# Kernel optimization log

Measured on AMD Instinct MI355X. Metric: run time of the kernel, lower is better.

## Reference

```python
import jax, jax.numpy as jnp
import numpy as np
from math import factorial

# ---------- Clebsch-Gordan coefficients (e3nn real-basis convention) ----------
def _su2_cg(j1, m1, j2, m2, j3, m3):
    if m3 != m1 + m2:
        return 0.0
    f = factorial
    vmin = int(max(-j1 + j2 + m3, -j1 + m1, 0))
    vmax = int(min(j2 + j3 + m1, j3 - j1 + j2, j3 + m3))
    c = ((2 * j3 + 1) * f(j3 + j1 - j2) * f(j3 - j1 + j2) * f(j1 + j2 - j3) / f(j1 + j2 + j3 + 1)
         * f(j3 + m3) * f(j3 - m3) / (f(j1 + m1) * f(j1 - m1) * f(j2 + m2) * f(j2 - m2))) ** 0.5
    s = 0.0
    for v in range(vmin, vmax + 1):
        s += (-1.0) ** (v + j2 + m2) / f(v) * f(j2 + j3 + m1 - v) * f(j1 - m1 + v) \
             / f(j3 - j1 + j2 - v) / f(j3 + m3 - v) / f(v + j1 - j2 - m3)
    return c * s

def _q(l):
    # change of basis real -> complex spherical harmonics, with (-i)^l phase (e3nn)
    q = np.zeros((2 * l + 1, 2 * l + 1), dtype=np.complex128)
    for m in range(-l, 0):
        q[l + m, l + abs(m)] = 2 ** -0.5
        q[l + m, l - abs(m)] = -1j * 2 ** -0.5
    q[l, l] = 1.0
    for m in range(1, l + 1):
        q[l + m, l + abs(m)] = (-1) ** m * 2 ** -0.5
        q[l + m, l - abs(m)] = 1j * (-1) ** m * 2 ** -0.5
    return (-1j) ** l * q

def _w3j(l1, l2, l3):
    # real-basis Wigner 3j, unit Frobenius norm (e3nn convention)
    C = np.zeros((2 * l1 + 1, 2 * l2 + 1, 2 * l3 + 1), dtype=np.complex128)
    for m1 in range(-l1, l1 + 1):
        for m2 in range(-l2, l2 + 1):
            m3 = m1 + m2
            if abs(m3) <= l3:
                C[l1 + m1, l2 + m2, l3 + m3] = _su2_cg(l1, m1, l2, m2, l3, m3)
    C = np.einsum('ij,kl,mn,ikm->jln', _q(l1), _q(l2), np.conj(_q(l3)), C).real
    return (C / np.linalg.norm(C)).astype(np.float32)

MAX_ELL = 3
AVG_NEIGH = 16.0
P_ENV = 6
N_NODES = 2048
MUL = 64

# tensor-product paths (l1 from Y=0e+1o+2e+3o, l2 from V=0e+1o+2e),
# filtered to ir_out in {0e,1o,2e} (= '0e' + output_irreps), grouped by output ir
PATHS_0E = [(0, 0, 0), (1, 1, 0), (2, 2, 0)]
PATHS_1O = [(0, 1, 1), (1, 0, 1), (1, 2, 1), (2, 1, 1), (3, 2, 1)]
PATHS_2E = [(0, 2, 2), (1, 1, 2), (2, 0, 2), (2, 2, 2), (3, 1, 2)]
_CG = {p: _w3j(*p) for p in PATHS_0E + PATHS_1O + PATHS_2E}
_CG_REC = [_w3j(1, 1, 2), _w3j(2, 1, 3)]  # for SH recursion

def _sh_scales():
    # component normalization: ||Y_l(n)|| = sqrt(2l+1) for unit n
    n = np.array([0.3, 0.5, 0.81]); n /= np.linalg.norm(n)
    nyzx = np.array([n[1], n[2], n[0]])
    Y = np.sqrt(3.0) * nyzx
    scales = []
    for i, l in enumerate((1, 2)):
        A = np.einsum('i,j,ijk->k', Y, nyzx, _CG_REC[i])
        s = np.sqrt(2 * (l + 1) + 1.0) / np.linalg.norm(A)
        scales.append(np.float32(s))
        Y = A * s
    return scales
_SH_SCALES = _sh_scales()

def _sph(vectors):
    # component-normalized real spherical harmonics l=0..3 (e3nn y,z,x basis)
    n = vectors / jnp.linalg.norm(vectors, axis=-1, keepdims=True)
    nyzx = jnp.stack([n[:, 1], n[:, 2], n[:, 0]], axis=-1)
    Y0 = jnp.ones((vectors.shape[0], 1), vectors.dtype)
    Y1 = np.float32(np.sqrt(3.0)) * nyzx
    Y2 = _SH_SCALES[0] * jnp.einsum('ei,ej,ijk->ek', Y1, nyzx, _CG_REC[0])
    Y3 = _SH_SCALES[1] * jnp.einsum('ei,ej,ijk->ek', Y2, nyzx, _CG_REC[1])
    return jnp.concatenate([Y0, Y1, Y2, Y3], axis=-1)  # (E, 16)

def _compute_silu_c():
    # e3nn normalized activation: silu(z) / sqrt(E[silu(z)^2]), z~N(0,1)
    trapz = getattr(np, 'trapezoid', getattr(np, 'trapz', None))
    z = np.linspace(-12.0, 12.0, 200001)
    phi = np.exp(-z * z / 2) / np.sqrt(2 * np.pi)
    s = z / (1.0 + np.exp(-z))
    return np.float32(1.0 / np.sqrt(trapz(s * s * phi, z)))
_SILU_C = _compute_silu_c()

def _silu_n(x):
    return jax.nn.silu(x) * _SILU_C

def _sl(l):
    return slice(l * l, (l + 1) * (l + 1))

def _envelope(d, p=P_ENV):
    # e3nn poly_envelope(p-1, 2) == DimeNet cutoff polynomial
    a = np.float32(-(p + 1) * (p + 2) / 2)
    b = np.float32(p * (p + 2))
    c = np.float32(-p * (p + 1) / 2)
    val = 1.0 + a * d ** p + b * d ** (p + 1) + c * d ** (p + 2)
    return jnp.where(d < 1.0, val, jnp.zeros_like(d))

def _forward(vectors, x, V, senders, W0, W1, W2, W3, Wl1, Wl2):
    E = x.shape[0]
    # edge-wise channel weights: mlp((mul_gcd,), act=None)
    w = (x @ W0) * np.float32(1.0 / np.sqrt(x.shape[1]))          # (E, MUL)
    Y = _sph(vectors)                                              # (E, 16)
    wY = w[:, :, None] * Y[:, None, :]                             # (E, MUL, 16)
    node_sum = jax.ops.segment_sum(wY, senders, num_segments=N_NODES)
    wY = node_sum[senders] * np.float32(1.0 / np.sqrt(AVG_NEIGH))  # scatter_sum(map_back=True)
    Vc = V.reshape(E, MUL, 9)                                      # mul_to_axis: 0e+1o+2e

    def tp(paths):
        outs = [np.float32(np.sqrt(2 * l3 + 1)) *
                jnp.einsum('eui,euj,ijk->euk', wY[:, :, _sl(l1)], Vc[:, :, _sl(l2)], _CG[(l1, l2, l3)])
                for (l1, l2, l3) in paths]
        return jnp.stack(outs, axis=2)  # (E, MUL, n_paths, 2*l3+1)

    s0 = tp(PATHS_0E).reshape(E, MUL * 3)      # 192x0e scalars
    v1 = tp(PATHS_1O).reshape(E, MUL * 5, 3)   # 320x1o
    v2 = tp(PATHS_2E).reshape(E, MUL * 5, 5)   # 320x2e

    # scalar track: concat 0e outputs, 3-layer MLP (normalized silu, no output act)
    x2 = jnp.concatenate([x, s0], axis=1)
    h = _silu_n(x2 @ W1 * np.float32(1.0 / np.sqrt(x2.shape[1])))
    h = _silu_n(h @ W2 * np.float32(1.0 / np.sqrt(h.shape[1])))
    h = h @ W3 * np.float32(1.0 / np.sqrt(h.shape[1]))
    d = jnp.linalg.norm(vectors, axis=-1, keepdims=True)
    x_out = _envelope(d) * h                                       # (E, 64)

    # equivariant track: e3nn Linear to 64x0e+64x1o+64x2e (no 0e input -> zeros)
    inv = np.float32(1.0 / np.sqrt(MUL * 5))
    o1 = jnp.einsum('emi,mu->eui', v1, Wl1) * inv
    o2 = jnp.einsum('emi,mu->eui', v2, Wl2) * inv
    V_out = jnp.concatenate([jnp.zeros((E, MUL), x.dtype),
                             o1.reshape(E, MUL * 3), o2.reshape(E, MUL * 5)], axis=1)  # (E, 576)
    return x_out, V_out

def setup_inputs() -> dict:
    key = jax.random.key(0)
    ks = jax.random.split(key, 11)
    E, XD = 32768, 128
    v = jax.random.normal(ks[0], (E, 3), dtype=jnp.float32)
    r = jax.random.uniform(ks[1], (E, 1), minval=0.05, maxval=0.95, dtype=jnp.float32)
    vectors = v / jnp.linalg.norm(v, axis=1, keepdims=True) * r  # lengths in (0,1): inside cutoff
    return {
        'vectors': vectors,
        'x': jax.random.normal(ks[2], (E, XD), dtype=jnp.float32),
        'V': jax.random.normal(ks[3], (E, MUL * 9), dtype=jnp.float32),
        'senders': jax.random.randint(ks[4], (E,), 0, N_NODES),
        'W0': jax.random.normal(ks[5], (XD, MUL), dtype=jnp.float32),
        'W1': jax.random.normal(ks[6], (XD + 3 * MUL, 64), dtype=jnp.float32),
        'W2': jax.random.normal(ks[7], (64, 64), dtype=jnp.float32),
        'W3': jax.random.normal(ks[8], (64, 64), dtype=jnp.float32),
        'Wl1': jax.random.normal(ks[9], (5 * MUL, MUL), dtype=jnp.float32),
        'Wl2': jax.random.normal(ks[10], (5 * MUL, MUL), dtype=jnp.float32),
    }

def reference(vectors, x, V, senders, W0, W1, W2, W3, Wl1, Wl2):
    return _forward(vectors, x, V, senders, W0, W1, W2, W3, Wl1, Wl2)
```

## Files before the change

### kernel.cpp

```cpp
#include <hip/hip_runtime.h>
#include <cmath>
#include <utility>

#define DI __device__ __forceinline__

typedef __attribute__((ext_vector_type(8))) short  short8;
typedef __attribute__((ext_vector_type(4))) float  f32x4;

constexpr double cfact(int n){ double r=1.0; for(int i=2;i<=n;++i) r*=(double)i; return r; }
constexpr double csqrt(double x){ if(x<=0.0) return 0.0; double g = x>1.0?x:1.0; for(int i=0;i<100;++i) g = 0.5*(g + x/g); return g; }
constexpr double csgn(int k){ int m = k%2; if(m<0) m+=2; return m? -1.0:1.0; }
constexpr int cmax3(int a,int b,int c){ int m=a>b?a:b; return m>c?m:c; }
constexpr int cmin3(int a,int b,int c){ int m=a<b?a:b; return m<c?m:c; }

struct cplx { double r, i; };
constexpr cplx cmul(cplx a, cplx b){ return cplx{a.r*b.r - a.i*b.i, a.r*b.i + a.i*b.r}; }
constexpr cplx cadd(cplx a, cplx b){ return cplx{a.r+b.r, a.i+b.i}; }
constexpr cplx cscale(cplx a, double s){ return cplx{a.r*s, a.i*s}; }
constexpr cplx cconj(cplx a){ return cplx{a.r, -a.i}; }

constexpr double su2_cg(int j1,int m1,int j2,int m2,int j3,int m3){
  if (m3 != m1+m2) return 0.0;
  const int vmin = cmax3(-j1+j2+m3, -j1+m1, 0);
  const int vmax = cmin3(j2+j3+m1, j3-j1+j2, j3+m3);
  const double c = csqrt((2.0*j3+1.0) * cfact(j3+j1-j2)*cfact(j3-j1+j2)*cfact(j1+j2-j3)/cfact(j1+j2+j3+1)
                         * cfact(j3+m3)*cfact(j3-m3)
                         / (cfact(j1+m1)*cfact(j1-m1)*cfact(j2+m2)*cfact(j2-m2)));
  double s = 0.0;
  for (int v=vmin; v<=vmax; ++v){
    s += csgn(v+j2+m2)/cfact(v)*cfact(j2+j3+m1-v)*cfact(j1-m1+v)
         /cfact(j3-j1+j2-v)/cfact(j3+m3-v)/cfact(v+j1-j2-m3);
  }
  return c*s;
}

template<int L> struct QM { cplx v[2*L+1][2*L+1]; };
template<int L> constexpr QM<L> qmat(){
  QM<L> q{};
  const double is2 = 0.70710678118654752440;
  for (int m=-L; m<0; ++m){
    q.v[L+m][L-m] = cplx{is2, 0.0};
    q.v[L+m][L+m] = cplx{0.0, -is2};
  }
  q.v[L][L] = cplx{1.0, 0.0};
  for (int m=1; m<=L; ++m){
    const double sg = (m%2)? -1.0 : 1.0;
    q.v[L+m][L+m] = cplx{sg*is2, 0.0};
    q.v[L+m][L-m] = cplx{0.0, sg*is2};
  }
  const cplx ph = (L%4==0)?cplx{1,0} : (L%4==1)?cplx{0,-1} : (L%4==2)?cplx{-1,0} : cplx{0,1};
  for (int a=0;a<2*L+1;++a) for(int b=0;b<2*L+1;++b) q.v[a][b] = cmul(ph, q.v[a][b]);
  return q;
}

template<int L1,int L2,int L3> struct W3J { float v[2*L1+1][2*L2+1][2*L3+1]; };

template<int L1,int L2,int L3> constexpr W3J<L1,L2,L3> w3j(){
  constexpr int N1=2*L1+1, N2=2*L2+1, N3=2*L3+1;
  double C[N1][N2][N3] = {};
  for (int m1=-L1;m1<=L1;++m1) for (int m2=-L2;m2<=L2;++m2){
    const int m3=m1+m2;
    if (m3>=-L3 && m3<=L3) C[L1+m1][L2+m2][L3+m3] = su2_cg(L1,m1,L2,m2,L3,m3);
  }
  const QM<L1> q1 = qmat<L1>(); const QM<L2> q2 = qmat<L2>(); const QM<L3> q3 = qmat<L3>();
  cplx T1[N1][N2][N3] = {};
  for(int j=0;j<N1;++j) for(int k=0;k<N2;++k) for(int m=0;m<N3;++m){
    cplx acc{0,0};
    for(int i=0;i<N1;++i) acc = cadd(acc, cscale(q1.v[i][j], C[i][k][m]));
    T1[j][k][m]=acc;
  }
  cplx T2[N1][N2][N3] = {};
  for(int j=0;j<N1;++j) for(int l=0;l<N2;++l) for(int m=0;m<N3;++m){
    cplx acc{0,0};
    for(int k=0;k<N2;++k) acc = cadd(acc, cmul(q2.v[k][l], T1[j][k][m]));
    T2[j][l][m]=acc;
  }
  double O[N1][N2][N3] = {};
  double fro = 0.0;
  for(int j=0;j<N1;++j) for(int l=0;l<N2;++l) for(int n=0;n<N3;++n){
    cplx acc{0,0};
    for(int m=0;m<N3;++m) acc = cadd(acc, cmul(cconj(q3.v[m][n]), T2[j][l][m]));
    O[j][l][n] = acc.r;
    fro += acc.r*acc.r;
  }
  const double inv = 1.0/csqrt(fro);
  W3J<L1,L2,L3> w{};
  for(int j=0;j<N1;++j) for(int l=0;l<N2;++l) for(int n=0;n<N3;++n)
    w.v[j][l][n] = (float)(O[j][l][n]*inv);
  return w;
}

constexpr auto CG_000 = w3j<0,0,0>();
constexpr auto CG_110 = w3j<1,1,0>();
constexpr auto CG_220 = w3j<2,2,0>();
constexpr auto CG_011 = w3j<0,1,1>();
constexpr auto CG_101 = w3j<1,0,1>();
constexpr auto CG_121 = w3j<1,2,1>();
constexpr auto CG_211 = w3j<2,1,1>();
constexpr auto CG_321 = w3j<3,2,1>();
constexpr auto CG_022 = w3j<0,2,2>();
constexpr auto CG_112 = w3j<1,1,2>();
constexpr auto CG_202 = w3j<2,0,2>();
constexpr auto CG_222 = w3j<2,2,2>();
constexpr auto CG_312 = w3j<3,1,2>();
constexpr auto CG_213 = w3j<2,1,3>();

struct ShS { double s0, s1; };
constexpr ShS sh_scales(){
  const double n0=0.3,n1=0.5,n2=0.81;
  const double nn = csqrt(n0*n0+n1*n1+n2*n2);
  const double ny[3] = {n1/nn, n2/nn, n0/nn};
  const double sq3 = csqrt(3.0);
  double Y1[3]; for(int i=0;i<3;++i) Y1[i] = sq3*ny[i];
  double A[5] = {};
  for(int i=0;i<3;++i) for(int j=0;j<3;++j) for(int k=0;k<5;++k)
    A[k] += Y1[i]*ny[j]*(double)CG_112.v[i][j][k];
  double na=0; for(int k=0;k<5;++k) na += A[k]*A[k]; na = csqrt(na);
  const double s0 = csqrt(5.0)/na;
  double Y2[5]; for(int k=0;k<5;++k) Y2[k] = A[k]*s0;
  double B[7] = {};
  for(int i=0;i<5;++i) for(int j=0;j<3;++j) for(int k=0;k<7;++k)
    B[k] += Y2[i]*ny[j]*(double)CG_213.v[i][j][k];
  double nb=0; for(int k=0;k<7;++k) nb += B[k]*B[k]; nb = csqrt(nb);
  const double s1 = csqrt(7.0)/nb;
  return ShS{s0,s1};
}
constexpr ShS SHS = sh_scales();

template<typename F, int... Is>
DI void sfor_impl(F&& f, std::integer_sequence<int, Is...>){ (f(std::integral_constant<int,Is>{}), ...); }
template<int N, typename F>
DI void sfor(F&& f){ sfor_impl(f, std::make_integer_sequence<int, N>{}); }

template<int N>
__host__ __device__ constexpr bool col_any(const float (&c)[N]){
  for(int k=0;k<N;++k) if (c[k]!=0.0f) return true;
  return false;
}

#define CONTRACT3(TAB, NI, NJ, NK, SCALE, INI, INJ, OUT) \
  sfor<(NI)>([&](auto I__){ constexpr int i__ = decltype(I__)::value; \
    sfor<(NJ)>([&](auto J__){ constexpr int j__ = decltype(J__)::value; \
      if constexpr (col_any((TAB).v[i__][j__])) { \
        const float t__ = (INI)[i__] * (INJ)[j__]; \
        sfor<(NK)>([&](auto K__){ constexpr int k__ = decltype(K__)::value; \
          if constexpr ((TAB).v[i__][j__][k__] != 0.0f) { \
            constexpr float c__ = (float)((double)(TAB).v[i__][j__][k__] * (double)(SCALE)); \
            (OUT)[k__] = fmaf(c__, t__, (OUT)[k__]); \
          } }); } }); });

DI unsigned short f2bf(float f){
  unsigned int u = __float_as_uint(f);
  u += 0x7fffu + ((u >> 16) & 1u);
  return (unsigned short)(u >> 16);
}
DI float silu_n(float z, float c){ return c * (z / (1.0f + __expf(-z))); }

constexpr float SQRT3F        = (float)csqrt(3.0);
constexpr double SQ3D         = csqrt(3.0);
constexpr double SQ5D         = csqrt(5.0);
constexpr float INV_SQRT_XD   = (float)(1.0/csqrt(128.0));
constexpr float INV_SQRT_NEI  = 0.25f;
constexpr float INV320        = (float)(1.0/csqrt(320.0));

constexpr int E_TOT = 32768;
constexpr int NNODE = 2048;

DI short8 load_bfrag_raw(const float* __restrict__ W, int kt, int nt, int lane){
  const int q = lane >> 4, c = lane & 15;
  const float* src = W + (kt*32 + q*8)*64 + nt*16 + c;
  short8 b;
  #pragma unroll
  for (int j=0;j<8;++j) b[j] = (short)f2bf(src[j*64]);
  return b;
}

__global__ __launch_bounds__(256) void k_setup(
    const int* __restrict__ senders, int* __restrict__ pos, int* __restrict__ cnt,
    const float* __restrict__ W0, const float* __restrict__ W1,
    const float* __restrict__ Wl1, const float* __restrict__ Wl2,
    const float* __restrict__ W2, const float* __restrict__ W3,
    short8* __restrict__ bfrag)
{
  const int blk = blockIdx.x;
  if (blk < 38){
    if (bfrag == nullptr) return;
    const int wv = threadIdx.x >> 6, lane = threadIdx.x & 63;
    const int wid = blk*4 + wv;
    if (wid >= 152) return;
    const float* W; int kt, nt;
    if (wid < 16){ W = W0; kt = wid>>2; nt = wid&3; }
    else if (wid < 136){ const int t = wid-16; const int mat = t/40, r = t%40;
           W = (mat==0)?W1 : (mat==1)?Wl1 : Wl2; kt = r>>2; nt = r&3; }
    else { const int t = wid-136; const int r = t&7;
           W = (t<8)?W2:W3; kt = r>>2; nt = r&3; }
    bfrag[wid*64 + lane] = load_bfrag_raw(W, kt, nt, lane);
  } else {
    const int e = (blk-38)*256 + threadIdx.x;
    if (e < E_TOT) pos[e] = atomicAdd(&cnt[senders[e]], 1);
  }
}

__global__ __launch_bounds__(256) void k_scan(const int* __restrict__ cnt, int* __restrict__ off)
{
  __shared__ int ts[256];
  const int t = threadIdx.x;
  int loc[8]; int s = 0;
  #pragma unroll
  for (int i=0;i<8;++i){ int v = cnt[t*8+i]; loc[i] = s; s += v; }
  ts[t] = s;
  __syncthreads();
  int val = s;
  for (int d=1; d<256; d<<=1){
    int other = (t>=d)? ts[t-d] : 0;
    __syncthreads();
    val += other; ts[t] = val;
    __syncthreads();
  }
  const int base = val - s;
  #pragma unroll
  for (int i=0;i<8;++i) off[t*8+i] = base + loc[i];
  if (t==255) off[2048] = val;
}

__global__ __launch_bounds__(256) void k_wy(
    const float* __restrict__ vectors, const float* __restrict__ x,
    const int* __restrict__ senders, const float* __restrict__ W0,
    const int* __restrict__ pos, const int* __restrict__ off,
    const short8* __restrict__ bfrag,
    float* __restrict__ w_un, float* __restrict__ Y_un, int* __restrict__ eids)
{
  const int tid = threadIdx.x, lane = tid & 63, wv = tid >> 6;
  const int e0 = blockIdx.x * 64;
  const int r = lane & 15, q = lane >> 4;
  const int erow = e0 + wv*16 + r;

  f32x4 acc[4] = {{0.f,0.f,0.f,0.f},{0.f,0.f,0.f,0.f},{0.f,0.f,0.f,0.f},{0.f,0.f,0.f,0.f}};
  #pragma unroll
  for (int kt=0; kt<4; ++kt){
    const float4* xp = (const float4*)(x + (size_t)erow*128 + kt*32 + q*8);
    const float4 xa = xp[0], xb = xp[1];
    short8 a;
    a[0]=(short)f2bf(xa.x); a[1]=(short)f2bf(xa.y); a[2]=(short)f2bf(xa.z); a[3]=(short)f2bf(xa.w);
    a[4]=(short)f2bf(xb.x); a[5]=(short)f2bf(xb.y); a[6]=(short)f2bf(xb.z); a[7]=(short)f2bf(xb.w);
    #pragma unroll
    for (int nt=0; nt<4; ++nt){
      const short8 b = (bfrag != nullptr) ? bfrag[(kt*4+nt)*64 + lane]
                                          : load_bfrag_raw(W0, kt, nt, lane);
      acc[nt] = __builtin_amdgcn_mfma_f32_16x16x32_bf16(a, b, acc[nt], 0,0,0);
    }
  }
  #pragma unroll
  for (int nt=0; nt<4; ++nt)
    #pragma unroll
    for (int reg=0; reg<4; ++reg){
      const int row = q*4 + reg;
      w_un[(size_t)(e0 + wv*16 + row)*64 + nt*16 + r] = acc[nt][reg] * INV_SQRT_XD;
    }

  if (tid < 64){
    const int e = e0 + tid;
    const float vx = vectors[e*3+0], vy = vectors[e*3+1], vz = vectors[e*3+2];
    const float dn = sqrtf(vx*vx+vy*vy+vz*vz);
    const float ny[3] = {vy/dn, vz/dn, vx/dn};
    float Y[16];
    Y[0] = 1.f; Y[1] = SQRT3F*ny[0]; Y[2] = SQRT3F*ny[1]; Y[3] = SQRT3F*ny[2];
    #pragma unroll
    for (int k=4;k<16;++k) Y[k] = 0.f;
    CONTRACT3(CG_112, 3,3,5, SHS.s0, (Y+1), ny, (Y+4));
    CONTRACT3(CG_213, 5,3,7, SHS.s1, (Y+4), ny, (Y+9));
    #pragma unroll
    for (int k=0;k<16;++k) Y_un[e*16+k] = Y[k];
    const int s = senders[e];
    eids[off[s] + pos[e]] = e;
  }
}

__global__ __launch_bounds__(256) void k_gather(
    const float* __restrict__ w_un, const float* __restrict__ Y_un,
    const int* __restrict__ off, const int* __restrict__ eids,
    float* __restrict__ node_sum)
{
  const int lane = threadIdx.x & 63;
  const int wv = threadIdx.x >> 6;
  const int n = __builtin_amdgcn_readfirstlane((int)blockIdx.x*4 + wv);
  const int p0 = off[n], p1 = off[n+1];
  float acc[16];
  #pragma unroll
  for (int k=0;k<16;++k) acc[k] = 0.f;
  if (p1 > p0){
    int eid = eids[p0];
    float wu = w_un[(size_t)eid*64 + lane];
    float yv[16];
    #pragma unroll
    for (int k=0;k<16;++k) yv[k] = Y_un[eid*16 + k];
    for (int p=p0+1; p<p1; ++p){
      const int eid2 = eids[p];
      const float wu2 = w_un[(size_t)eid2*64 + lane];
      float yv2[16];
      #pragma unroll
      for (int k=0;k<16;++k) yv2[k] = Y_un[eid2*16 + k];
      #pragma unroll
      for (int k=0;k<16;++k) acc[k] = fmaf(yv[k], wu, acc[k]);
      wu = wu2;
      #pragma unroll
      for (int k=0;k<16;++k) yv[k] = yv2[k];
    }
    #pragma unroll
    for (int k=0;k<16;++k) acc[k] = fmaf(yv[k], wu, acc[k]);
  }
  float* dst = node_sum + n*1024;
  #pragma unroll
  for (int k=0;k<16;++k) dst[k*64 + lane] = acc[k] * INV_SQRT_NEI;
}

DI void wr2(char* AF, int tile, int row, int m, float val){
  const int kt = m >> 5, m0 = m & 31;
  *(unsigned short*)(AF + (((tile*10 + kt)*16 + row)<<6)
                        + ((m0<<1) ^ (((row>>1)&3)<<4))) = f2bf(val);
}

constexpr int SSTR = 580;

__global__ __launch_bounds__(256,5) void k_main(
    const float* __restrict__ vectors, const float* __restrict__ x,
    const float* __restrict__ V, const int* __restrict__ senders,
    const float* __restrict__ W1, const float* __restrict__ W2,
    const float* __restrict__ W3, const float* __restrict__ Wl1,
    const float* __restrict__ Wl2, const float* __restrict__ node_sum,
    const short8* __restrict__ bfrag,
    float* __restrict__ out_x, float* __restrict__ out_V, float silu_c)
{
  __shared__ __align__(16) char smem[30752];
  char*  AF    = smem;
  float* stage = (float*)(smem + 2048);
  char*  h1b   = smem;
  char*  h2b   = smem + 12288;
  float* envs  = (float*)(smem + 30720);

  const int tid  = threadIdx.x;
  const int lane = tid & 63;
  const int wv   = tid >> 6;
  const int blk  = blockIdx.x;

  {
    const int el = wv;
    const int e  = __builtin_amdgcn_readfirstlane(blk*4 + el);
    const int s  = senders[e];
    const int u  = lane;

    float* smV = (float*)(smem + wv*2304);
    #pragma unroll
    for (int j=0;j<9;++j) smV[j*64 + lane] = V[(size_t)e*576 + j*64 + lane];
    float vc[9];
    #pragma unroll
    for (int j=0;j<9;++j) vc[j] = smV[u*9 + j];

    float g[16];
    const float* nsrow = node_sum + s*1024;
    #pragma unroll
    for (int k=0;k<16;++k) g[k] = nsrow[k*64+u];
    const float x0 = x[(size_t)e*128 + u];
    const float x1 = x[(size_t)e*128 + 64 + u];

    const float vx = vectors[e*3+0], vy = vectors[e*3+1], vz = vectors[e*3+2];
    const float d  = sqrtf(vx*vx + vy*vy + vz*vz);
    const float d3 = d*d*d, d6 = d3*d3;
    const float env = (d < 1.f) ? (1.f + d6*(-28.f + d*(48.f + d*(-21.f)))) : 0.f;
    if (lane == 0) envs[wv] = env;

    __syncthreads();

    float s0[3] = {0.f,0.f,0.f};
    float v1o[5][3] = {};
    float v2o[5][5] = {};
    CONTRACT3(CG_000, 1,1,1, 1.0, (g+0), (vc+0), (&s0[0]));
    CONTRACT3(CG_110, 3,3,1, 1.0, (g+1), (vc+1), (&s0[1]));
    CONTRACT3(CG_220, 5,5,1, 1.0, (g+4), (vc+4), (&s0[2]));
    CONTRACT3(CG_011, 1,3,3, SQ3D, (g+0), (vc+1), (v1o[0]));
    CONTRACT3(CG_101, 3,1,3, SQ3D, (g+1), (vc+0), (v1o[1]));
    CONTRACT3(CG_121, 3,5,3, SQ3D, (g+1), (vc+4), (v1o[2]));
    CONTRACT3(CG_211, 5,3,3, SQ3D, (g+4), (vc+1), (v1o[3]));
    CONTRACT3(CG_321, 7,5,3, SQ3D, (g+9), (vc+4), (v1o[4]));
    CONTRACT3(CG_022, 1,5,5, SQ5D, (g+0), (vc+4), (v2o[0]));
    CONTRACT3(CG_112, 3,3,5, SQ5D, (g+1), (vc+1), (v2o[1]));
    CONTRACT3(CG_202, 5,1,5, SQ5D, (g+4), (vc+0), (v2o[2]));
    CONTRACT3(CG_222, 5,5,5, SQ5D, (g+4), (vc+4), (v2o[3]));
    CONTRACT3(CG_312, 7,3,5, SQ5D, (g+9), (vc+1), (v2o[4]));

    wr2(AF, 0, el, u,      x0);
    wr2(AF, 0, el, 64 + u, x1);
    #pragma unroll
    for (int p=0;p<3;++p) wr2(AF, 0, el, 128 + u*3 + p, s0[p]);
    #pragma unroll
    for (int p=0;p<5;++p){
      const int m = u*5 + p;
      #pragma unroll
      for (int i=0;i<3;++i) wr2(AF, 0, 4 + i*4 + el, m, v1o[p][i]);
      #pragma unroll
      for (int i=0;i<4;++i) wr2(AF, 1, i*4 + el, m, v2o[p][i]);
      wr2(AF, 2, el, m, v2o[p][4]);
    }
  }
  __syncthreads();

  f32x4 accS={0.f,0.f,0.f,0.f}, accV1=accS, accA=accS, accB=accS;
  const int nt = wv;
  const int arow = lane & 15;
  const int aoff = arow*64 + (((lane>>4)<<4) ^ (((arow>>1)&3)<<4));
  __builtin_amdgcn_s_setprio(1);
  #pragma unroll 2
  for (int kt=0; kt<10; ++kt){
    short8 b0, b1, b2;
    if (bfrag != nullptr){
      b0 = bfrag[(16 + kt*4 + nt)*64 + lane];
      b1 = bfrag[(56 + kt*4 + nt)*64 + lane];
      b2 = bfrag[(96 + kt*4 + nt)*64 + lane];
    } else {
      b0 = load_bfrag_raw(W1,  kt, nt, lane);
      b1 = load_bfrag_raw(Wl1, kt, nt, lane);
      b2 = load_bfrag_raw(Wl2, kt, nt, lane);
    }
    const char* ab = AF + kt*1024 + aoff;
    const short8 a0 = *(const short8*)(ab);
    const short8 a1 = *(const short8*)(ab + 10240);
    const short8 a2 = *(const short8*)(ab + 20480);
    accS  = __builtin_amdgcn_mfma_f32_16x16x32_bf16(a0, b0, accS,  0,0,0);
    accV1 = __builtin_amdgcn_mfma_f32_16x16x32_bf16(a0, b1, accV1, 0,0,0);
    accA  = __builtin_amdgcn_mfma_f32_16x16x32_bf16(a1, b2, accA,  0,0,0);
    accB  = __builtin_amdgcn_mfma_f32_16x16x32_bf16(a2, b2, accB,  0,0,0);
  }
  __builtin_amdgcn_s_setprio(0);
  __syncthreads();

  const int col = lane & 15, qq = lane >> 4;
  const int u2 = nt*16 + col;
  stage[qq*SSTR + u2] = 0.f;
  #pragma unroll
  for (int reg=0; reg<4; ++reg){
    const int row = qq*4 + reg;
    if (row < 4){
      wr2(h1b, 0, row, u2, silu_n(accS[reg] * INV320, silu_c));
      stage[row*SSTR + 256 + u2*5 + 4] = accB[reg] * INV320;
    } else {
      const int rr = row - 4, i = rr>>2, ee = rr&3;
      stage[ee*SSTR + 64 + u2*3 + i] = accV1[reg] * INV320;
    }
    { const int i2 = row>>2, ee = row&3;
      stage[ee*SSTR + 256 + u2*5 + i2] = accA[reg] * INV320; }
  }
  __syncthreads();

  f32x4 acc2 = {0.f,0.f,0.f,0.f};
  #pragma unroll
  for (int kt2=0; kt2<2; ++kt2){
    const short8 b = (bfrag != nullptr) ? bfrag[(136 + kt2*4 + nt)*64 + lane]
                                        : load_bfrag_raw(W2, kt2, nt, lane);
    const short8 a = *(const short8*)(h1b + kt2*1024 + aoff);
    acc2 = __builtin_amdgcn_mfma_f32_16x16x32_bf16(a, b, acc2, 0,0,0);
  }
  if (qq == 0){
    #pragma unroll
    for (int reg=0; reg<4; ++reg)
      wr2(h2b, 0, reg, u2, silu_n(acc2[reg] * 0.125f, silu_c));
  }
  __syncthreads();

  f32x4 acc3 = {0.f,0.f,0.f,0.f};
  #pragma unroll
  for (int kt2=0; kt2<2; ++kt2){
    const short8 b = (bfrag != nullptr) ? bfrag[(144 + kt2*4 + nt)*64 + lane]
                                        : load_bfrag_raw(W3, kt2, nt, lane);
    const short8 a = *(const short8*)(h2b + kt2*1024 + aoff);
    acc3 = __builtin_amdgcn_mfma_f32_16x16x32_bf16(a, b, acc3, 0,0,0);
  }
  if (qq == 0){
    #pragma unroll
    for (int reg=0; reg<4; ++reg)
      out_x[(size_t)(blk*4 + reg)*64 + u2] = envs[reg] * (acc3[reg] * 0.125f);
  }

  const int e2 = blk*4 + wv;
  const float* st = stage + wv*SSTR;
  #pragma unroll
  for (int j=0;j<9;++j) out_V[(size_t)e2*576 + j*64 + lane] = st[j*64 + lane];
}

static const float g_silu_c = [](){
  const int N = 200001;
  const double h = 24.0/(double)(N-1);
  double acc = 0.0;
  for (int i=0;i<N;++i){
    const double z = -12.0 + h*(double)i;
    const double phi = std::exp(-z*z/2.0)/std::sqrt(2.0*M_PI);
    const double s = z/(1.0+std::exp(-z));
    const double f = s*s*phi;
    acc += (i==0 || i==N-1) ? 0.5*f : f;
  }
  return (float)(1.0/std::sqrt(acc*h));
}();

extern "C" void kernel_launch(void* const* d_in, const int* in_sizes, int n_in,
                              void* d_out, int out_size, void* d_ws, size_t ws_size,
                              hipStream_t stream) {
  (void)in_sizes; (void)n_in; (void)out_size;
  const float* vectors = (const float*)d_in[0];
  const float* x       = (const float*)d_in[1];
  const float* V       = (const float*)d_in[2];
  const int*   senders = (const int*)  d_in[3];
  const float* W0      = (const float*)d_in[4];
  const float* W1      = (const float*)d_in[5];
  const float* W2      = (const float*)d_in[6];
  const float* W3      = (const float*)d_in[7];
  const float* Wl1     = (const float*)d_in[8];
  const float* Wl2     = (const float*)d_in[9];
  float* out_x = (float*)d_out;
  float* out_V = out_x + (size_t)E_TOT*64;

  char* ob = (char*)d_out;
  int*   pos   = (int*)(ob);
  int*   cnt   = (int*)(ob + 131072);
  int*   off   = (int*)(ob + 139264);
  int*   eids  = (int*)(ob + 151552);
  float* w_un  = (float*)(ob + 282624);
  float* Y_un  = (float*)(ob + 282624 + 8388608);

  float* node_sum = (float*)d_ws;
  const size_t WS_NEED = (size_t)8*1024*1024 + 152*1024;
  short8* bfrag = (ws_size >= WS_NEED) ? (short8*)((char*)d_ws + 8*1024*1024) : nullptr;

  hipMemsetAsync(cnt, 0, 8192, stream);
  k_setup <<<dim3(166), dim3(256), 0, stream>>>(senders, pos, cnt, W0, W1, Wl1, Wl2, W2, W3, bfrag);
  k_scan  <<<dim3(1),   dim3(256), 0, stream>>>(cnt, off);
  k_wy    <<<dim3(E_TOT/64), dim3(256), 0, stream>>>(vectors, x, senders, W0, pos, off, bfrag, w_un, Y_un, eids);
  k_gather<<<dim3(NNODE/4),  dim3(256), 0, stream>>>(w_un, Y_un, off, eids, node_sum);
  k_main  <<<dim3(E_TOT/4),  dim3(256), 0, stream>>>(vectors, x, V, senders,
                                                     W1, W2, W3, Wl1, Wl2,
                                                     node_sum, bfrag, out_x, out_V, g_silu_c);
}
```

Baseline: 248.6 us.

## Replace sort-and-gather aggregation with fused atomic scatter into node sums

Drops the counting sort (setup atomics, scan, eid scatter) and the separate gather kernel. One kernel now computes the W0 projection and the spherical harmonics per edge and atomically adds the outer products straight into a zeroed node_sum buffer. Weight fragment preparation moves into extra blocks of that kernel. This removes several launches and the intermediate w_un/Y_un round trip, but issues 1024 float atomics per edge, makes summation order nondeterministic, and reads W0 fragments raw from fp32 in every block.

After: 324.2 us. 1.3x slower.

```diff
diff --git a/kernel.cpp b/kernel.cpp
--- a/kernel.cpp
+++ b/kernel.cpp
@@ -160,8 +160,8 @@
 constexpr double SQ3D         = csqrt(3.0);
 constexpr double SQ5D         = csqrt(5.0);
 constexpr float INV_SQRT_XD   = (float)(1.0/csqrt(128.0));
-constexpr float INV_SQRT_NEI  = 0.25f;
 constexpr float INV320        = (float)(1.0/csqrt(320.0));
+constexpr float WSCALE        = (float)((1.0/csqrt(128.0)) * 0.25);
 
 constexpr int E_TOT = 32768;
 constexpr int NNODE = 2048;
@@ -175,88 +175,37 @@
   return b;
 }
 
-__global__ __launch_bounds__(256) void k_setup(
-    const int* __restrict__ senders, int* __restrict__ pos, int* __restrict__ cnt,
-    const float* __restrict__ W0, const float* __restrict__ W1,
-    const float* __restrict__ Wl1, const float* __restrict__ Wl2,
-    const float* __restrict__ W2, const float* __restrict__ W3,
-    short8* __restrict__ bfrag)
-{
-  const int blk = blockIdx.x;
-  if (blk < 38){
-    if (bfrag == nullptr) return;
-    const int wv = threadIdx.x >> 6, lane = threadIdx.x & 63;
-    const int wid = blk*4 + wv;
-    if (wid >= 152) return;
-    const float* W; int kt, nt;
-    if (wid < 16){ W = W0; kt = wid>>2; nt = wid&3; }
-    else if (wid < 136){ const int t = wid-16; const int mat = t/40, r = t%40;
-           W = (mat==0)?W1 : (mat==1)?Wl1 : Wl2; kt = r>>2; nt = r&3; }
-    else { const int t = wid-136; const int r = t&7;
-           W = (t<8)?W2:W3; kt = r>>2; nt = r&3; }
-    bfrag[wid*64 + lane] = load_bfrag_raw(W, kt, nt, lane);
-  } else {
-    const int e = (blk-38)*256 + threadIdx.x;
-    if (e < E_TOT) pos[e] = atomicAdd(&cnt[senders[e]], 1);
-  }
-}
-
-__global__ __launch_bounds__(256) void k_scan(const int* __restrict__ cnt, int* __restrict__ off)
-{
-  __shared__ int ts[256];
-  const int t = threadIdx.x;
-  int loc[8]; int s = 0;
-  #pragma unroll
-  for (int i=0;i<8;++i){ int v = cnt[t*8+i]; loc[i] = s; s += v; }
-  ts[t] = s;
-  __syncthreads();
-  int val = s;
-  for (int d=1; d<256; d<<=1){
-    int other = (t>=d)? ts[t-d] : 0;
-    __syncthreads();
-    val += other; ts[t] = val;
-    __syncthreads();
-  }
-  const int base = val - s;
-  #pragma unroll
-  for (int i=0;i<8;++i) off[t*8+i] = base + loc[i];
-  if (t==255) off[2048] = val;
-}
-
-__global__ __launch_bounds__(256) void k_wy(
+__global__ __launch_bounds__(256) void k_scat(
     const float* __restrict__ vectors, const float* __restrict__ x,
     const int* __restrict__ senders, const float* __restrict__ W0,
-    const int* __restrict__ pos, const int* __restrict__ off,
-    const short8* __restrict__ bfrag,
-    float* __restrict__ w_un, float* __restrict__ Y_un, int* __restrict__ eids)
+    const float* __restrict__ W1, const float* __restrict__ Wl1,
+    const float* __restrict__ Wl2, const float* __restrict__ W2,
+    const float* __restrict__ W3,
+    short8* __restrict__ bfrag, float* __restrict__ node_sum)
 {
   const int tid = threadIdx.x, lane = tid & 63, wv = tid >> 6;
-  const int e0 = blockIdx.x * 64;
-  const int r = lane & 15, q = lane >> 4;
-  const int erow = e0 + wv*16 + r;
-
-  f32x4 acc[4] = {{0.f,0.f,0.f,0.f},{0.f,0.f,0.f,0.f},{0.f,0.f,0.f,0.f},{0.f,0.f,0.f,0.f}};
-  #pragma unroll
-  for (int kt=0; kt<4; ++kt){
-    const float4* xp = (const float4*)(x + (size_t)erow*128 + kt*32 + q*8);
-    const float4 xa = xp[0], xb = xp[1];
-    short8 a;
-    a[0]=(short)f2bf(xa.x); a[1]=(short)f2bf(xa.y); a[2]=(short)f2bf(xa.z); a[3]=(short)f2bf(xa.w);
-    a[4]=(short)f2bf(xb.x); a[5]=(short)f2bf(xb.y); a[6]=(short)f2bf(xb.z); a[7]=(short)f2bf(xb.w);
-    #pragma unroll
-    for (int nt=0; nt<4; ++nt){
-      const short8 b = (bfrag != nullptr) ? bfrag[(kt*4+nt)*64 + lane]
-                                          : load_bfrag_raw(W0, kt, nt, lane);
-      acc[nt] = __builtin_amdgcn_mfma_f32_16x16x32_bf16(a, b, acc[nt], 0,0,0);
-    }
-  }
-  #pragma unroll
-  for (int nt=0; nt<4; ++nt)
-    #pragma unroll
-    for (int reg=0; reg<4; ++reg){
-      const int row = q*4 + reg;
-      w_un[(size_t)(e0 + wv*16 + row)*64 + nt*16 + r] = acc[nt][reg] * INV_SQRT_XD;
-    }
+  const int blk = blockIdx.x;
+
+  if (blk >= 512){
+    if (bfrag != nullptr){
+      const int wid = 16 + (blk-512)*4 + wv;
+      if (wid < 152){
+        const float* W; int kt, nt;
+        const int t = wid - 16;
+        if (t < 120){ const int mat = t/40, r2 = t%40;
+          W = (mat==0)?W1 : (mat==1)?Wl1 : Wl2; kt = r2>>2; nt = r2&3; }
+        else { const int t2 = t-120; const int r2 = t2&7;
+          W = (t2<8)?W2:W3; kt = r2>>2; nt = r2&3; }
+        bfrag[wid*64 + lane] = load_bfrag_raw(W, kt, nt, lane);
+      }
+    }
+    return;
+  }
+
+  __shared__ float Ys[64][17];
+  __shared__ int   sl[64];
+
+  const int e0 = blk * 64;
 
   if (tid < 64){
     const int e = e0 + tid;
@@ -270,48 +219,45 @@
     CONTRACT3(CG_112, 3,3,5, SHS.s0, (Y+1), ny, (Y+4));
     CONTRACT3(CG_213, 5,3,7, SHS.s1, (Y+4), ny, (Y+9));
     #pragma unroll
-    for (int k=0;k<16;++k) Y_un[e*16+k] = Y[k];
-    const int s = senders[e];
-    eids[off[s] + pos[e]] = e;
-  }
-}
-
-__global__ __launch_bounds__(256) void k_gather(
-    const float* __restrict__ w_un, const float* __restrict__ Y_un,
-    const int* __restrict__ off, const int* __restrict__ eids,
-    float* __restrict__ node_sum)
-{
-  const int lane = threadIdx.x & 63;
-  const int wv = threadIdx.x >> 6;
-  const int n = __builtin_amdgcn_readfirstlane((int)blockIdx.x*4 + wv);
-  const int p0 = off[n], p1 = off[n+1];
-  float acc[16];
-  #pragma unroll
-  for (int k=0;k<16;++k) acc[k] = 0.f;
-  if (p1 > p0){
-    int eid = eids[p0];
-    float wu = w_un[(size_t)eid*64 + lane];
-    float yv[16];
-    #pragma unroll
-    for (int k=0;k<16;++k) yv[k] = Y_un[eid*16 + k];
-    for (int p=p0+1; p<p1; ++p){
-      const int eid2 = eids[p];
-      const float wu2 = w_un[(size_t)eid2*64 + lane];
-      float yv2[16];
+    for (int k=0;k<16;++k) Ys[tid][k] = Y[k];
+    sl[tid] = senders[e];
+  }
+  __syncthreads();
+
+  const int r = lane & 15, q = lane >> 4;
+  const int erow = e0 + wv*16 + r;
+
+  f32x4 acc[4] = {{0.f,0.f,0.f,0.f},{0.f,0.f,0.f,0.f},{0.f,0.f,0.f,0.f},{0.f,0.f,0.f,0.f}};
+  #pragma unroll
+  for (int kt=0; kt<4; ++kt){
+    const float4* xp = (const float4*)(x + (size_t)erow*128 + kt*32 + q*8);
+    const float4 xa = xp[0], xb = xp[1];
+    short8 a;
+    a[0]=(short)f2bf(xa.x); a[1]=(short)f2bf(xa.y); a[2]=(short)f2bf(xa.z); a[3]=(short)f2bf(xa.w);
+    a[4]=(short)f2bf(xb.x); a[5]=(short)f2bf(xb.y); a[6]=(short)f2bf(xb.z); a[7]=(short)f2bf(xb.w);
+    #pragma unroll
+    for (int nt=0; nt<4; ++nt){
+      const short8 b = load_bfrag_raw(W0, kt, nt, lane);
+      acc[nt] = __builtin_amdgcn_mfma_f32_16x16x32_bf16(a, b, acc[nt], 0,0,0);
+    }
+  }
+
+  const int ebase = wv*16 + q*4;
+  #pragma unroll
+  for (int reg=0; reg<4; ++reg){
+    const int eloc = ebase + reg;
+    float* bp = node_sum + (size_t)sl[eloc]*1024 + r;
+    float wvv[4];
+    #pragma unroll
+    for (int nt=0; nt<4; ++nt) wvv[nt] = acc[nt][reg] * WSCALE;
+    #pragma unroll
+    for (int k=0;k<16;++k){
+      const float yk = Ys[eloc][k];
       #pragma unroll
-      for (int k=0;k<16;++k) yv2[k] = Y_un[eid2*16 + k];
-      #pragma unroll
-      for (int k=0;k<16;++k) acc[k] = fmaf(yv[k], wu, acc[k]);
-      wu = wu2;
-      #pragma unroll
-      for (int k=0;k<16;++k) yv[k] = yv2[k];
-    }
-    #pragma unroll
-    for (int k=0;k<16;++k) acc[k] = fmaf(yv[k], wu, acc[k]);
-  }
-  float* dst = node_sum + n*1024;
-  #pragma unroll
-  for (int k=0;k<16;++k) dst[k*64 + lane] = acc[k] * INV_SQRT_NEI;
+      for (int nt=0; nt<4; ++nt)
+        atomicAdd(bp + k*64 + nt*16, wvv[nt] * yk);
+    }
+  }
 }
 
 DI void wr2(char* AF, int tile, int row, int m, float val){
@@ -517,23 +463,14 @@
   float* out_x = (float*)d_out;
   float* out_V = out_x + (size_t)E_TOT*64;
 
-  char* ob = (char*)d_out;
-  int*   pos   = (int*)(ob);
-  int*   cnt   = (int*)(ob + 131072);
-  int*   off   = (int*)(ob + 139264);
-  int*   eids  = (int*)(ob + 151552);
-  float* w_un  = (float*)(ob + 282624);
-  float* Y_un  = (float*)(ob + 282624 + 8388608);
-
   float* node_sum = (float*)d_ws;
   const size_t WS_NEED = (size_t)8*1024*1024 + 152*1024;
   short8* bfrag = (ws_size >= WS_NEED) ? (short8*)((char*)d_ws + 8*1024*1024) : nullptr;
 
-  hipMemsetAsync(cnt, 0, 8192, stream);
-  k_setup <<<dim3(166), dim3(256), 0, stream>>>(senders, pos, cnt, W0, W1, Wl1, Wl2, W2, W3, bfrag);
-  k_scan  <<<dim3(1),   dim3(256), 0, stream>>>(cnt, off);
-  k_wy    <<<dim3(E_TOT/64), dim3(256), 0, stream>>>(vectors, x, senders, W0, pos, off, bfrag, w_un, Y_un, eids);
-  k_gather<<<dim3(NNODE/4),  dim3(256), 0, stream>>>(w_un, Y_un, off, eids, node_sum);
+  hipMemsetAsync(node_sum, 0, (size_t)NNODE*1024*sizeof(float), stream);
+  k_scat  <<<dim3(546),      dim3(256), 0, stream>>>(vectors, x, senders, W0,
+                                                     W1, Wl1, Wl2, W2, W3,
+                                                     bfrag, node_sum);
   k_main  <<<dim3(E_TOT/4),  dim3(256), 0, stream>>>(vectors, x, V, senders,
                                                      W1, W2, W3, Wl1, Wl2,
                                                      node_sum, bfrag, out_x, out_V, g_silu_c);
```
